# Kernel tuning notes

Measured on AMD Instinct MI355X. Metric: run time of the kernel, lower is better.

Reference implementation:

```python
import jax, jax.numpy as jnp
import numpy as np


def _bilinear(plane, coords):
    # plane: [B, C, H, W]; coords: [B, N, 2] in [-1, 1]; coords[...,0]->x (W axis), [...,1]->y (H axis)
    # matches F.grid_sample(mode='bilinear', padding_mode='border', align_corners=True)
    B, C, H, W = plane.shape
    x = jnp.clip((coords[..., 0] + 1.0) * 0.5 * (W - 1), 0.0, W - 1)
    y = jnp.clip((coords[..., 1] + 1.0) * 0.5 * (H - 1), 0.0, H - 1)
    x0 = jnp.floor(x)
    y0 = jnp.floor(y)
    x0i = x0.astype(jnp.int32)
    y0i = y0.astype(jnp.int32)
    x1i = jnp.minimum(x0i + 1, W - 1)
    y1i = jnp.minimum(y0i + 1, H - 1)
    wx = (x - x0)[:, :, None]
    wy = (y - y0)[:, :, None]
    pf = plane.reshape(B, C, H * W)

    def g(yi, xi):
        idx = (yi * W + xi)[:, None, :]            # [B,1,N]
        return jnp.take_along_axis(pf, idx, axis=2).transpose(0, 2, 1)  # [B,N,C]

    f00 = g(y0i, x0i)
    f01 = g(y0i, x1i)
    f10 = g(y1i, x0i)
    f11 = g(y1i, x1i)
    return (f00 * (1 - wx) * (1 - wy) + f01 * wx * (1 - wy)
            + f10 * (1 - wx) * wy + f11 * wx * wy)


def _sample(p, c_xz, c_xy, c_yz):
    # project 3D points onto the three canonical planes and sum bilinear features
    return (_bilinear(c_xz, p[..., jnp.array([0, 2])])
            + _bilinear(c_xy, p[..., jnp.array([0, 1])])
            + _bilinear(c_yz, p[..., jnp.array([1, 2])]))


def setup_inputs() -> dict:
    key = jax.random.key(0)
    ks = jax.random.split(key, 10)
    B, N, C, S, H = 8, 4096, 128, 8, 64
    query_pos = jax.random.uniform(ks[0], (B, N, 3), dtype=jnp.float32) * 2.0 - 1.0
    c_xz = jax.random.normal(ks[1], (B, C, H, H), dtype=jnp.float32)
    c_xy = jax.random.normal(ks[2], (B, C, H, H), dtype=jnp.float32)
    c_yz = jax.random.normal(ks[3], (B, C, H, H), dtype=jnp.float32)
    s = C ** -0.5
    Wq = jax.random.normal(ks[4], (C, C), dtype=jnp.float32) * s
    Wk = jax.random.normal(ks[5], (C, C), dtype=jnp.float32) * s
    Wv = jax.random.normal(ks[6], (C, C), dtype=jnp.float32) * s
    Wout = jax.random.normal(ks[7], (C, C), dtype=jnp.float32) * s
    Woff = jax.random.normal(ks[8], (C, 3 * S), dtype=jnp.float32) * s * 0.1  # small offsets
    return dict(query_pos=query_pos, c_xz=c_xz, c_xy=c_xy, c_yz=c_yz,
                Wq=Wq, bq=jnp.zeros((C,), jnp.float32),
                Wk=Wk, bk=jnp.zeros((C,), jnp.float32),
                Wv=Wv, bv=jnp.zeros((C,), jnp.float32),
                Wout=Wout, bout=jnp.zeros((C,), jnp.float32),
                Woff=Woff, boff=jnp.zeros((3 * S,), jnp.float32))


def reference(query_pos, c_xz, c_xy, c_yz, Wq, bq, Wk, bk, Wv, bv,
              Wout, bout, Woff, boff):
    B, N, _ = query_pos.shape
    C = Wq.shape[0]
    S = Woff.shape[1] // 3
    # sample features at query points (bilinear gather from triplanes)
    feature = _sample(query_pos, c_xz, c_xy, c_yz)                     # [B,N,C]
    # learned deformable offsets -> S auxiliary sample points per query
    offset = (feature @ Woff + boff).reshape(B, N, S, 3)
    aux_pts = offset + query_pos[:, :, None, :]                        # [B,N,S,3]
    aux_feat = _sample(aux_pts.reshape(B, N * S, 3),
                       c_xz, c_xy, c_yz).reshape(B, N, S, C)           # [B,N,S,C]
    k = aux_feat @ Wk + bk                                             # [B,N,S,C]
    v = aux_feat @ Wv + bv
    q = feature @ Wq + bq                                              # [B,N,C]
    scale = C ** (-0.5)
    q = q / scale  # faithful to original: q = q / self.scale
    sim = jnp.einsum('bnd,bnjd->bnj', q, k)                            # [B,N,S]
    attn = jax.nn.softmax(sim, axis=-1)
    out = jnp.einsum('bnj,bnjd->bnd', attn, v)                         # [B,N,C]
    out = out @ Wout + bout + feature                                  # residual
    return out
```

## Files before the change

kernel.cpp:

```cpp
#include <hip/hip_runtime.h>
#include <math.h>

#define BB 8
#define NN 4096
#define CC 128
#define SS 8
#define HH 64
#define HW 4096
#define PLANE_B (HW*CC)
#define SQRT_C 11.3137084989847603904f

__global__ __launch_bounds__(128) void transpose_planes(
    const float* __restrict__ pxz, const float* __restrict__ pxy,
    const float* __restrict__ pyz, float* __restrict__ dst) {
  int bid = blockIdx.x;
  int c   = threadIdx.x;
  int hw0 = (bid & 255) * 16;
  int b   = (bid >> 8) & 7;
  int p   = bid >> 11;
  const float* src = (p == 0) ? pxz : (p == 1) ? pxy : pyz;
  const float4* s4 = (const float4*)(src + (size_t)(b * CC + c) * HW + hw0);
  float4 v0 = s4[0], v1 = s4[1], v2 = s4[2], v3 = s4[3];
  float vals[16];
  vals[0]=v0.x; vals[1]=v0.y; vals[2]=v0.z; vals[3]=v0.w;
  vals[4]=v1.x; vals[5]=v1.y; vals[6]=v1.z; vals[7]=v1.w;
  vals[8]=v2.x; vals[9]=v2.y; vals[10]=v2.z; vals[11]=v2.w;
  vals[12]=v3.x; vals[13]=v3.y; vals[14]=v3.z; vals[15]=v3.w;
  float* d = dst + (size_t)(p * BB + b) * PLANE_B + (size_t)hw0 * CC + c;
#pragma unroll
  for (int i = 0; i < 16; ++i) d[i * CC] = vals[i];
}

__global__ __launch_bounds__(128) void prep_mats(
    const float* __restrict__ Wq, const float* __restrict__ bq,
    const float* __restrict__ Wk,
    const float* __restrict__ Wv, const float* __restrict__ bv,
    const float* __restrict__ Wout, const float* __restrict__ bout,
    const float* __restrict__ Woff,
    float* __restrict__ Mt, float* __restrict__ u,
    float* __restrict__ W2, float* __restrict__ b2,
    float* __restrict__ Wofft) {
  int t = threadIdx.x;
  int blk = blockIdx.x;
  if (blk < 128) {
    __shared__ float lwq[128];
    lwq[t] = Wq[blk * 128 + t];
    __syncthreads();
    float acc = 0.f;
#pragma unroll 8
    for (int d = 0; d < 128; ++d) acc += Wk[t * 128 + d] * lwq[d];
    Mt[blk * 128 + t] = SQRT_C * acc;
  } else if (blk < 256) {
    int c = blk - 128;
    float acc = 0.f;
#pragma unroll 8
    for (int e = 0; e < 128; ++e) acc += Wv[c * 128 + e] * Wout[e * 128 + t];
    W2[c * 128 + t] = acc;
  } else if (blk == 256) {
    float au = 0.f, ab = 0.f;
    for (int d = 0; d < 128; ++d) au += Wk[t * 128 + d] * bq[d];
    u[t] = SQRT_C * au;
    for (int e = 0; e < 128; ++e) ab += bv[e] * Wout[e * 128 + t];
    b2[t] = ab + bout[t];
  } else {
#pragma unroll
    for (int j = 0; j < 24; ++j) Wofft[j * 128 + t] = Woff[t * 24 + j];
  }
}

__device__ __forceinline__ void make_combo(float cx, float cy,
                                           int4* oi, float4* ow) {
  float fx = fminf(fmaxf((cx + 1.f) * 31.5f, 0.f), 63.f);
  float fy = fminf(fmaxf((cy + 1.f) * 31.5f, 0.f), 63.f);
  float x0f = floorf(fx), y0f = floorf(fy);
  int x0 = (int)x0f, y0 = (int)y0f;
  int x1 = min(x0 + 1, 63), y1 = min(y0 + 1, 63);
  float wx = fx - x0f, wy = fy - y0f;
  int r0 = y0 << 15, r1 = y1 << 15;
  int cb0 = x0 << 9, cb1 = x1 << 9;
  *oi = make_int4(r0 + cb0, r0 + cb1, r1 + cb0, r1 + cb1);
  float wxy = wx * wy;
  *ow = make_float4(1.f - wx - wy + wxy, wx - wxy, wy - wxy, wxy);
}

__device__ __forceinline__ float ldf(const char* p, int off) {
  return *(const float*)(p + off);
}

__global__ __launch_bounds__(128, 4) void deform_attn3(
    const float* __restrict__ qpos, const float* __restrict__ pT,
    const float* __restrict__ Mt, const float* __restrict__ u,
    const float* __restrict__ W2, const float* __restrict__ bias2,
    const float* __restrict__ Wofft, const float* __restrict__ boff,
    float* __restrict__ out) {
  const int tid = threadIdx.x;
  const int c = tid;
  const int l = tid & 63;
  const int wv = tid >> 6;
  const int bid = blockIdx.x;
  const int b = bid & 7;
  const int n0 = (bid >> 3) * 8;

  __shared__ float spos[24];
  __shared__ int4   sfi[24];
  __shared__ float4 sfw[24];
  __shared__ int4   sci[192];
  __shared__ float4 scw[192];
  __shared__ __align__(16) float sfeat[CC * 8];
  __shared__ __align__(16) float swacc[CC * 8];
  __shared__ float soff[8][24];
  __shared__ float sred[8][2][8];

  if (tid < 24) spos[tid] = qpos[(size_t)(b * NN + n0) * 3 + tid];
  __syncthreads();

  const char* pb0 = (const char*)(pT + (size_t)(0 * BB + b) * PLANE_B + c);
  const char* pb1 = (const char*)(pT + (size_t)(1 * BB + b) * PLANE_B + c);
  const char* pb2 = (const char*)(pT + (size_t)(2 * BB + b) * PLANE_B + c);

  if (tid < 24) {
    int p = tid >> 3, q = tid & 7;
    float px = spos[q * 3 + 0], py = spos[q * 3 + 1], pz = spos[q * 3 + 2];
    float cx = (p == 2) ? py : px;
    float cy = (p == 1) ? py : pz;
    make_combo(cx, cy, &sfi[tid], &sfw[tid]);
  }
  __syncthreads();

  float featr[8];
#pragma unroll
  for (int q = 0; q < 8; ++q) {
    float f = 0.f;
#pragma unroll
    for (int p = 0; p < 3; ++p) {
      int4 oi = sfi[p * 8 + q];
      float4 w = sfw[p * 8 + q];
      const char* base = (p == 0) ? pb0 : (p == 1) ? pb1 : pb2;
      f += w.x * ldf(base, oi.x) + w.y * ldf(base, oi.y)
         + w.z * ldf(base, oi.z) + w.w * ldf(base, oi.w);
    }
    featr[q] = f;
    sfeat[c * 8 + q] = f;
  }
  __syncthreads();

  float qk[8];
  {
    float uc = u[c];
#pragma unroll
    for (int q = 0; q < 8; ++q) qk[q] = uc;
#pragma unroll 4
    for (int cp = 0; cp < CC; ++cp) {
      float m = Mt[cp * CC + c];
      float4 f0 = *(const float4*)&sfeat[cp * 8];
      float4 f1 = *(const float4*)&sfeat[cp * 8 + 4];
      qk[0] += m * f0.x; qk[1] += m * f0.y; qk[2] += m * f0.z; qk[3] += m * f0.w;
      qk[4] += m * f1.x; qk[5] += m * f1.y; qk[6] += m * f1.z; qk[7] += m * f1.w;
    }
  }

#pragma unroll
  for (int rep = 0; rep < 2; ++rep) {
    int m = rep * 128 + tid;
    if (m < 192) {
      int q = m / 24;
      int t24 = m - q * 24;
      float acc = boff[t24];
      const float* wrow = Wofft + t24 * 128;
#pragma unroll 4
      for (int cp = 0; cp < CC; ++cp) acc += sfeat[cp * 8 + q] * wrow[cp];
      soff[q][t24] = acc;
    }
  }
  __syncthreads();

#pragma unroll
  for (int rep = 0; rep < 2; ++rep) {
    int m = rep * 128 + tid;
    if (m < 192) {
      int p = m >> 6, q = (m >> 3) & 7, j = m & 7;
      float ox = spos[q * 3 + 0] + soff[q][j * 3 + 0];
      float oy = spos[q * 3 + 1] + soff[q][j * 3 + 1];
      float oz = spos[q * 3 + 2] + soff[q][j * 3 + 2];
      float cx = (p == 2) ? oy : ox;
      float cy = (p == 1) ? oy : oz;
      make_combo(cx, cy, &sci[m], &scw[m]);
    }
  }
  __syncthreads();

  const int lb0 = l & 1, lb1 = (l >> 1) & 1, lb2 = (l >> 2) & 1;
#pragma unroll
  for (int q = 0; q < 8; ++q) {
    float a8[8], part[8];
#pragma unroll
    for (int j = 0; j < 8; ++j) {
      float a = 0.f;
#pragma unroll
      for (int p = 0; p < 3; ++p) {
        int idx = p * 64 + q * 8 + j;
        int4 oi = sci[idx];
        float4 w = scw[idx];
        const char* base = (p == 0) ? pb0 : (p == 1) ? pb1 : pb2;
        a += w.x * ldf(base, oi.x) + w.y * ldf(base, oi.y)
           + w.z * ldf(base, oi.z) + w.w * ldf(base, oi.w);
      }
      a8[j] = a;
      part[j] = a * qk[q];
    }
    float s2[4];
#pragma unroll
    for (int k = 0; k < 4; ++k) {
      float pa = part[2 * k], pb_ = part[2 * k + 1];
      float snd = lb0 ? pa : pb_;
      float kp  = lb0 ? pb_ : pa;
      s2[k] = kp + __shfl_xor(snd, 1);
    }
    float s4[2];
#pragma unroll
    for (int k = 0; k < 2; ++k) {
      float pa = s2[2 * k], pb_ = s2[2 * k + 1];
      float snd = lb1 ? pa : pb_;
      float kp  = lb1 ? pb_ : pa;
      s4[k] = kp + __shfl_xor(snd, 2);
    }
    float s8;
    {
      float snd = lb2 ? s4[0] : s4[1];
      float kp  = lb2 ? s4[1] : s4[0];
      s8 = kp + __shfl_xor(snd, 4);
    }
    s8 += __shfl_xor(s8, 8);
    s8 += __shfl_xor(s8, 16);
    s8 += __shfl_xor(s8, 32);
    if (l < 8) sred[q][wv][l] = s8;
    __syncthreads();
    float sim[8];
#pragma unroll
    for (int j = 0; j < 8; ++j) sim[j] = sred[q][0][j] + sred[q][1][j];
    float mx = fmaxf(fmaxf(fmaxf(sim[0], sim[1]), fmaxf(sim[2], sim[3])),
                     fmaxf(fmaxf(sim[4], sim[5]), fmaxf(sim[6], sim[7])));
    float den = 0.f;
#pragma unroll
    for (int j = 0; j < 8; ++j) { sim[j] = __expf(sim[j] - mx); den += sim[j]; }
    float inv = 1.f / den;
    float w = 0.f;
#pragma unroll
    for (int j = 0; j < 8; ++j) w += sim[j] * a8[j];
    swacc[c * 8 + q] = w * inv;
  }
  __syncthreads();

  float o[8];
  {
    float bb = bias2[c];
#pragma unroll
    for (int q = 0; q < 8; ++q) o[q] = bb;
#pragma unroll 4
    for (int cp = 0; cp < CC; ++cp) {
      float m = W2[cp * CC + c];
      float4 f0 = *(const float4*)&swacc[cp * 8];
      float4 f1 = *(const float4*)&swacc[cp * 8 + 4];
      o[0] += m * f0.x; o[1] += m * f0.y; o[2] += m * f0.z; o[3] += m * f0.w;
      o[4] += m * f1.x; o[5] += m * f1.y; o[6] += m * f1.z; o[7] += m * f1.w;
    }
  }
#pragma unroll
  for (int q = 0; q < 8; ++q) {
    out[(size_t)(b * NN + n0 + q) * CC + c] = o[q] + featr[q];
  }
}

__device__ __forceinline__ float bil(const float* __restrict__ base,
                                     float cx, float cy, int es, int rs) {
  float fx = fminf(fmaxf((cx + 1.f) * 31.5f, 0.f), 63.f);
  float fy = fminf(fmaxf((cy + 1.f) * 31.5f, 0.f), 63.f);
  float x0f = floorf(fx), y0f = floorf(fy);
  int x0 = (int)x0f, y0 = (int)y0f;
  int x1 = min(x0 + 1, 63), y1 = min(y0 + 1, 63);
  float wx = fx - x0f, wy = fy - y0f;
  const float* r0 = base + y0 * rs;
  const float* r1 = base + y1 * rs;
  float f00 = r0[x0 * es], f01 = r0[x1 * es];
  float f10 = r1[x0 * es], f11 = r1[x1 * es];
  float top = f00 + (f01 - f00) * wx;
  float bot = f10 + (f11 - f10) * wx;
  return top + (bot - top) * wy;
}

__global__ __launch_bounds__(128) void deform_attn_fb(
    const float* __restrict__ qpos,
    const float* __restrict__ pxz, const float* __restrict__ pxy,
    const float* __restrict__ pyz,
    const float* __restrict__ Mt, const float* __restrict__ u,
    const float* __restrict__ W2, const float* __restrict__ b2,
    const float* __restrict__ Woff, const float* __restrict__ boff,
    float* __restrict__ out) {
  const int tid = threadIdx.x;
  const int c = tid;
  const int bid = blockIdx.x;
  const int b = bid & 7;
  const int n0 = (bid >> 3) * 8;
  const int es = 1, rs = HH;
  const float* bxz = pxz + (size_t)(b * CC + c) * HW;
  const float* bxy = pxy + (size_t)(b * CC + c) * HW;
  const float* byz = pyz + (size_t)(b * CC + c) * HW;

  __shared__ __align__(16) float sfeat[CC * 8];
  __shared__ __align__(16) float swv[CC * 8];
  __shared__ float spos[24];
  __shared__ float soff[8][24];
  __shared__ float sred[8][2][8];

  if (tid < 24) spos[tid] = qpos[(size_t)(b * NN + n0) * 3 + tid];
  __syncthreads();
#pragma unroll
  for (int q = 0; q < 8; ++q) {
    float px = spos[q*3+0], py = spos[q*3+1], pz = spos[q*3+2];
    sfeat[c*8+q] = bil(bxz,px,pz,es,rs)+bil(bxy,px,py,es,rs)+bil(byz,py,pz,es,rs);
  }
  __syncthreads();
  float qk[8];
  {
    float uc = u[c];
#pragma unroll
    for (int q = 0; q < 8; ++q) qk[q] = uc;
    for (int cp = 0; cp < CC; ++cp) {
      float m = Mt[cp*CC+c];
#pragma unroll
      for (int q = 0; q < 8; ++q) qk[q] += m * sfeat[cp*8+q];
    }
  }
  if (tid < 120) {
    int q = tid/24, j = tid%24;
    float acc = boff[j];
    for (int cp = 0; cp < CC; ++cp) acc += sfeat[cp*8+q]*Woff[cp*24+j];
    soff[q][j] = acc;
  }
  if (tid < 72) {
    int q = 5+tid/24, j = tid%24;
    float acc = boff[j];
    for (int cp = 0; cp < CC; ++cp) acc += sfeat[cp*8+q]*Woff[cp*24+j];
    soff[q][j] = acc;
  }
  __syncthreads();
  const int wvid = tid >> 6;
  for (int q = 0; q < 8; ++q) {
    float px = spos[q*3+0], py = spos[q*3+1], pz = spos[q*3+2];
    float a8[8];
#pragma unroll
    for (int j = 0; j < 8; ++j) {
      float ox = px+soff[q][j*3+0], oy = py+soff[q][j*3+1], oz = pz+soff[q][j*3+2];
      float a = bil(bxz,ox,oz,es,rs)+bil(bxy,ox,oy,es,rs)+bil(byz,oy,oz,es,rs);
      a8[j] = a;
      float p = a * qk[q];
#pragma unroll
      for (int m = 1; m < 64; m <<= 1) p += __shfl_xor(p, m);
      if ((tid & 63) == 0) sred[q][wvid][j] = p;
    }
    __syncthreads();
    float attn[8], mx = -INFINITY;
#pragma unroll
    for (int j = 0; j < 8; ++j) { attn[j] = sred[q][0][j]+sred[q][1][j]; mx = fmaxf(mx, attn[j]); }
    float den = 0.f;
#pragma unroll
    for (int j = 0; j < 8; ++j) { attn[j] = __expf(attn[j]-mx); den += attn[j]; }
    float inv = 1.f/den, w = 0.f;
#pragma unroll
    for (int j = 0; j < 8; ++j) w += attn[j]*a8[j];
    swv[c*8+q] = w*inv;
  }
  __syncthreads();
  float o[8];
  {
    float bb = b2[c];
#pragma unroll
    for (int q = 0; q < 8; ++q) o[q] = bb;
    for (int cp = 0; cp < CC; ++cp) {
      float wv2 = W2[cp*CC+c];
#pragma unroll
      for (int q = 0; q < 8; ++q) o[q] += wv2 * swv[cp*8+q];
    }
  }
#pragma unroll
  for (int q = 0; q < 8; ++q)
    out[(size_t)(b*NN+n0+q)*CC+c] = o[q] + sfeat[c*8+q];
}

extern "C" void kernel_launch(void* const* d_in, const int* in_sizes, int n_in,
                              void* d_out, int out_size, void* d_ws, size_t ws_size,
                              hipStream_t stream) {
  const float* qpos = (const float*)d_in[0];
  const float* pxz  = (const float*)d_in[1];
  const float* pxy  = (const float*)d_in[2];
  const float* pyz  = (const float*)d_in[3];
  const float* Wq   = (const float*)d_in[4];
  const float* bq   = (const float*)d_in[5];
  const float* Wk   = (const float*)d_in[6];
  const float* Wv   = (const float*)d_in[8];
  const float* bv   = (const float*)d_in[9];
  const float* Wout = (const float*)d_in[10];
  const float* bout = (const float*)d_in[11];
  const float* Woff = (const float*)d_in[12];
  const float* boff = (const float*)d_in[13];
  float* out = (float*)d_out;

  float* w = (float*)d_ws;
  const size_t nT = (size_t)3 * BB * HW * CC;
  const size_t matFloats = 16384 + 128 + 16384 + 128 + 24 * 128;
  bool tp = ws_size >= (nT + matFloats) * sizeof(float);

  float* wsT  = w;
  float* wsMt = tp ? (w + nT) : w;
  float* wsU  = wsMt + 16384;
  float* wsW2 = wsU + 128;
  float* wsB2 = wsW2 + 16384;
  float* wsWofft = wsB2 + 128;

  prep_mats<<<258, 128, 0, stream>>>(Wq, bq, Wk, Wv, bv, Wout, bout, Woff,
                                     wsMt, wsU, wsW2, wsB2, wsWofft);
  if (tp) {
    transpose_planes<<<3 * BB * (HW / 16), 128, 0, stream>>>(pxz, pxy, pyz, wsT);
    deform_attn3<<<(BB * NN) / 8, 128, 0, stream>>>(
        qpos, wsT, wsMt, wsU, wsW2, wsB2, wsWofft, boff, out);
  } else {
    deform_attn_fb<<<(BB * NN) / 8, 128, 0, stream>>>(
        qpos, pxz, pxy, pyz, wsMt, wsU, wsW2, wsB2, Woff, boff, out);
  }
}
```

Before: 209.9 us.

## Split queries across waves with float2 channel gathers and in-wave softmax

The main kernel now has each wave handle 4 of the 8 queries, with each lane loading two adjacent channels as a float2 per bilinear corner. This halves the number of gather instructions and removes the per-query block barrier, since the softmax is now done entirely with intra-wave shuffles. qk values are staged through shared memory to match the new lane-to-channel layout. The Woff transpose in the prep kernel is dropped and Woff is read directly with strided access. The risks are extra shared-memory traffic and per-lane register pressure from holding two channel accumulators.

```diff
diff --git a/kernel.cpp b/kernel.cpp
--- a/kernel.cpp
+++ b/kernel.cpp
@@ -36,10 +36,8 @@
     const float* __restrict__ Wk,
     const float* __restrict__ Wv, const float* __restrict__ bv,
     const float* __restrict__ Wout, const float* __restrict__ bout,
-    const float* __restrict__ Woff,
     float* __restrict__ Mt, float* __restrict__ u,
-    float* __restrict__ W2, float* __restrict__ b2,
-    float* __restrict__ Wofft) {
+    float* __restrict__ W2, float* __restrict__ b2) {
   int t = threadIdx.x;
   int blk = blockIdx.x;
   if (blk < 128) {
@@ -56,15 +54,12 @@
 #pragma unroll 8
     for (int e = 0; e < 128; ++e) acc += Wv[c * 128 + e] * Wout[e * 128 + t];
     W2[c * 128 + t] = acc;
-  } else if (blk == 256) {
+  } else {
     float au = 0.f, ab = 0.f;
     for (int d = 0; d < 128; ++d) au += Wk[t * 128 + d] * bq[d];
     u[t] = SQRT_C * au;
     for (int e = 0; e < 128; ++e) ab += bv[e] * Wout[e * 128 + t];
     b2[t] = ab + bout[t];
-  } else {
-#pragma unroll
-    for (int j = 0; j < 24; ++j) Wofft[j * 128 + t] = Woff[t * 24 + j];
   }
 }
 
@@ -83,20 +78,21 @@
   *ow = make_float4(1.f - wx - wy + wxy, wx - wxy, wy - wxy, wxy);
 }
 
-__device__ __forceinline__ float ldf(const char* p, int off) {
-  return *(const float*)(p + off);
-}
-
-__global__ __launch_bounds__(128, 4) void deform_attn3(
+__device__ __forceinline__ float2 ld2(const char* p, int off) {
+  return *(const float2*)(p + off);
+}
+
+__global__ __launch_bounds__(128, 4) void deform_attn4(
     const float* __restrict__ qpos, const float* __restrict__ pT,
     const float* __restrict__ Mt, const float* __restrict__ u,
     const float* __restrict__ W2, const float* __restrict__ bias2,
-    const float* __restrict__ Wofft, const float* __restrict__ boff,
+    const float* __restrict__ Woff, const float* __restrict__ boff,
     float* __restrict__ out) {
   const int tid = threadIdx.x;
   const int c = tid;
   const int l = tid & 63;
   const int wv = tid >> 6;
+  const int qb = wv * 4;
   const int bid = blockIdx.x;
   const int b = bid & 7;
   const int n0 = (bid >> 3) * 8;
@@ -109,14 +105,13 @@
   __shared__ __align__(16) float sfeat[CC * 8];
   __shared__ __align__(16) float swacc[CC * 8];
   __shared__ float soff[8][24];
-  __shared__ float sred[8][2][8];
 
   if (tid < 24) spos[tid] = qpos[(size_t)(b * NN + n0) * 3 + tid];
   __syncthreads();
 
-  const char* pb0 = (const char*)(pT + (size_t)(0 * BB + b) * PLANE_B + c);
-  const char* pb1 = (const char*)(pT + (size_t)(1 * BB + b) * PLANE_B + c);
-  const char* pb2 = (const char*)(pT + (size_t)(2 * BB + b) * PLANE_B + c);
+  const char* gp0 = (const char*)(pT + (size_t)(0 * BB + b) * PLANE_B) + 8 * l;
+  const char* gp1 = (const char*)(pT + (size_t)(1 * BB + b) * PLANE_B) + 8 * l;
+  const char* gp2 = (const char*)(pT + (size_t)(2 * BB + b) * PLANE_B) + 8 * l;
 
   if (tid < 24) {
     int p = tid >> 3, q = tid & 7;
@@ -127,26 +122,33 @@
   }
   __syncthreads();
 
-  float featr[8];
-#pragma unroll
-  for (int q = 0; q < 8; ++q) {
-    float f = 0.f;
-#pragma unroll
-    for (int p = 0; p < 3; ++p) {
-      int4 oi = sfi[p * 8 + q];
-      float4 w = sfw[p * 8 + q];
-      const char* base = (p == 0) ? pb0 : (p == 1) ? pb1 : pb2;
-      f += w.x * ldf(base, oi.x) + w.y * ldf(base, oi.y)
-         + w.z * ldf(base, oi.z) + w.w * ldf(base, oi.w);
-    }
-    featr[q] = f;
-    sfeat[c * 8 + q] = f;
-  }
-  __syncthreads();
-
-  float qk[8];
+  {
+    float f0q[4], f1q[4];
+#pragma unroll
+    for (int qi = 0; qi < 4; ++qi) {
+      int q = qb + qi;
+      float f0 = 0.f, f1 = 0.f;
+#pragma unroll
+      for (int p = 0; p < 3; ++p) {
+        const char* g = (p == 0) ? gp0 : (p == 1) ? gp1 : gp2;
+        int4 oi = sfi[p * 8 + q];
+        float4 w = sfw[p * 8 + q];
+        float2 v;
+        v = ld2(g, oi.x); f0 += w.x * v.x; f1 += w.x * v.y;
+        v = ld2(g, oi.y); f0 += w.y * v.x; f1 += w.y * v.y;
+        v = ld2(g, oi.z); f0 += w.z * v.x; f1 += w.z * v.y;
+        v = ld2(g, oi.w); f0 += w.w * v.x; f1 += w.w * v.y;
+      }
+      f0q[qi] = f0; f1q[qi] = f1;
+    }
+    *(float4*)&sfeat[(2 * l) * 8 + qb]     = make_float4(f0q[0], f0q[1], f0q[2], f0q[3]);
+    *(float4*)&sfeat[(2 * l + 1) * 8 + qb] = make_float4(f1q[0], f1q[1], f1q[2], f1q[3]);
+  }
+  __syncthreads();
+
   {
     float uc = u[c];
+    float qk[8];
 #pragma unroll
     for (int q = 0; q < 8; ++q) qk[q] = uc;
 #pragma unroll 4
@@ -157,6 +159,8 @@
       qk[0] += m * f0.x; qk[1] += m * f0.y; qk[2] += m * f0.z; qk[3] += m * f0.w;
       qk[4] += m * f1.x; qk[5] += m * f1.y; qk[6] += m * f1.z; qk[7] += m * f1.w;
     }
+    *(float4*)&swacc[c * 8]     = make_float4(qk[0], qk[1], qk[2], qk[3]);
+    *(float4*)&swacc[c * 8 + 4] = make_float4(qk[4], qk[5], qk[6], qk[7]);
   }
 
 #pragma unroll
@@ -166,9 +170,8 @@
       int q = m / 24;
       int t24 = m - q * 24;
       float acc = boff[t24];
-      const float* wrow = Wofft + t24 * 128;
 #pragma unroll 4
-      for (int cp = 0; cp < CC; ++cp) acc += sfeat[cp * 8 + q] * wrow[cp];
+      for (int cp = 0; cp < CC; ++cp) acc += sfeat[cp * 8 + q] * Woff[cp * 24 + t24];
       soff[q][t24] = acc;
     }
   }
@@ -189,71 +192,87 @@
   }
   __syncthreads();
 
-  const int lb0 = l & 1, lb1 = (l >> 1) & 1, lb2 = (l >> 2) & 1;
-#pragma unroll
-  for (int q = 0; q < 8; ++q) {
-    float a8[8], part[8];
-#pragma unroll
-    for (int j = 0; j < 8; ++j) {
-      float a = 0.f;
-#pragma unroll
-      for (int p = 0; p < 3; ++p) {
-        int idx = p * 64 + q * 8 + j;
-        int4 oi = sci[idx];
-        float4 w = scw[idx];
-        const char* base = (p == 0) ? pb0 : (p == 1) ? pb1 : pb2;
-        a += w.x * ldf(base, oi.x) + w.y * ldf(base, oi.y)
-           + w.z * ldf(base, oi.z) + w.w * ldf(base, oi.w);
-      }
-      a8[j] = a;
-      part[j] = a * qk[q];
-    }
-    float s2[4];
-#pragma unroll
-    for (int k = 0; k < 4; ++k) {
-      float pa = part[2 * k], pb_ = part[2 * k + 1];
-      float snd = lb0 ? pa : pb_;
-      float kp  = lb0 ? pb_ : pa;
-      s2[k] = kp + __shfl_xor(snd, 1);
-    }
-    float s4[2];
-#pragma unroll
-    for (int k = 0; k < 2; ++k) {
-      float pa = s2[2 * k], pb_ = s2[2 * k + 1];
-      float snd = lb1 ? pa : pb_;
-      float kp  = lb1 ? pb_ : pa;
-      s4[k] = kp + __shfl_xor(snd, 2);
-    }
-    float s8;
-    {
-      float snd = lb2 ? s4[0] : s4[1];
-      float kp  = lb2 ? s4[1] : s4[0];
-      s8 = kp + __shfl_xor(snd, 4);
-    }
-    s8 += __shfl_xor(s8, 8);
-    s8 += __shfl_xor(s8, 16);
-    s8 += __shfl_xor(s8, 32);
-    if (l < 8) sred[q][wv][l] = s8;
-    __syncthreads();
-    float sim[8];
-#pragma unroll
-    for (int j = 0; j < 8; ++j) sim[j] = sred[q][0][j] + sred[q][1][j];
-    float mx = fmaxf(fmaxf(fmaxf(sim[0], sim[1]), fmaxf(sim[2], sim[3])),
-                     fmaxf(fmaxf(sim[4], sim[5]), fmaxf(sim[6], sim[7])));
-    float den = 0.f;
-#pragma unroll
-    for (int j = 0; j < 8; ++j) { sim[j] = __expf(sim[j] - mx); den += sim[j]; }
-    float inv = 1.f / den;
-    float w = 0.f;
-#pragma unroll
-    for (int j = 0; j < 8; ++j) w += sim[j] * a8[j];
-    swacc[c * 8 + q] = w * inv;
-  }
-  __syncthreads();
-
-  float o[8];
+  {
+    float4 qk0 = *(const float4*)&swacc[(2 * l) * 8 + qb];
+    float4 qk1 = *(const float4*)&swacc[(2 * l + 1) * 8 + qb];
+    const int lb0 = l & 1, lb1 = (l >> 1) & 1, lb2 = (l >> 2) & 1;
+    float w0q[4], w1q[4];
+#pragma unroll
+    for (int qi = 0; qi < 4; ++qi) {
+      int q = qb + qi;
+      float qv0 = (qi == 0) ? qk0.x : (qi == 1) ? qk0.y : (qi == 2) ? qk0.z : qk0.w;
+      float qv1 = (qi == 0) ? qk1.x : (qi == 1) ? qk1.y : (qi == 2) ? qk1.z : qk1.w;
+      float a0[8], a1[8], part[8];
+#pragma unroll
+      for (int j = 0; j < 8; ++j) {
+        float s0 = 0.f, s1 = 0.f;
+#pragma unroll
+        for (int p = 0; p < 3; ++p) {
+          int idx = p * 64 + q * 8 + j;
+          const char* g = (p == 0) ? gp0 : (p == 1) ? gp1 : gp2;
+          int4 oi = sci[idx];
+          float4 w = scw[idx];
+          float2 v;
+          v = ld2(g, oi.x); s0 += w.x * v.x; s1 += w.x * v.y;
+          v = ld2(g, oi.y); s0 += w.y * v.x; s1 += w.y * v.y;
+          v = ld2(g, oi.z); s0 += w.z * v.x; s1 += w.z * v.y;
+          v = ld2(g, oi.w); s0 += w.w * v.x; s1 += w.w * v.y;
+        }
+        a0[j] = s0; a1[j] = s1;
+        part[j] = s0 * qv0 + s1 * qv1;
+      }
+      float s2[4];
+#pragma unroll
+      for (int k = 0; k < 4; ++k) {
+        float pa = part[2 * k], pb_ = part[2 * k + 1];
+        float snd = lb0 ? pa : pb_;
+        float kp  = lb0 ? pb_ : pa;
+        s2[k] = kp + __shfl_xor(snd, 1);
+      }
+      float s4_[2];
+#pragma unroll
+      for (int k = 0; k < 2; ++k) {
+        float pa = s2[2 * k], pb_ = s2[2 * k + 1];
+        float snd = lb1 ? pa : pb_;
+        float kp  = lb1 ? pb_ : pa;
+        s4_[k] = kp + __shfl_xor(snd, 2);
+      }
+      float s8;
+      {
+        float snd = lb2 ? s4_[0] : s4_[1];
+        float kp  = lb2 ? s4_[1] : s4_[0];
+        s8 = kp + __shfl_xor(snd, 4);
+      }
+      s8 += __shfl_xor(s8, 8);
+      s8 += __shfl_xor(s8, 16);
+      s8 += __shfl_xor(s8, 32);
+      float mx = s8;
+      mx = fmaxf(mx, __shfl_xor(mx, 1));
+      mx = fmaxf(mx, __shfl_xor(mx, 2));
+      mx = fmaxf(mx, __shfl_xor(mx, 4));
+      float e = __expf(s8 - mx);
+      float den = e;
+      den += __shfl_xor(den, 1);
+      den += __shfl_xor(den, 2);
+      den += __shfl_xor(den, 4);
+      float attn = e / den;
+      float w0 = 0.f, w1 = 0.f;
+#pragma unroll
+      for (int j = 0; j < 8; ++j) {
+        float aj = __shfl(attn, j);
+        w0 += aj * a0[j];
+        w1 += aj * a1[j];
+      }
+      w0q[qi] = w0; w1q[qi] = w1;
+    }
+    *(float4*)&swacc[(2 * l) * 8 + qb]     = make_float4(w0q[0], w0q[1], w0q[2], w0q[3]);
+    *(float4*)&swacc[(2 * l + 1) * 8 + qb] = make_float4(w1q[0], w1q[1], w1q[2], w1q[3]);
+  }
+  __syncthreads();
+
   {
     float bb = bias2[c];
+    float o[8];
 #pragma unroll
     for (int q = 0; q < 8; ++q) o[q] = bb;
 #pragma unroll 4
@@ -264,10 +283,16 @@
       o[0] += m * f0.x; o[1] += m * f0.y; o[2] += m * f0.z; o[3] += m * f0.w;
       o[4] += m * f1.x; o[5] += m * f1.y; o[6] += m * f1.z; o[7] += m * f1.w;
     }
-  }
-#pragma unroll
-  for (int q = 0; q < 8; ++q) {
-    out[(size_t)(b * NN + n0 + q) * CC + c] = o[q] + featr[q];
+    float4 r0 = *(const float4*)&sfeat[c * 8];
+    float4 r1 = *(const float4*)&sfeat[c * 8 + 4];
+    out[(size_t)(b * NN + n0 + 0) * CC + c] = o[0] + r0.x;
+    out[(size_t)(b * NN + n0 + 1) * CC + c] = o[1] + r0.y;
+    out[(size_t)(b * NN + n0 + 2) * CC + c] = o[2] + r0.z;
+    out[(size_t)(b * NN + n0 + 3) * CC + c] = o[3] + r0.w;
+    out[(size_t)(b * NN + n0 + 4) * CC + c] = o[4] + r1.x;
+    out[(size_t)(b * NN + n0 + 5) * CC + c] = o[5] + r1.y;
+    out[(size_t)(b * NN + n0 + 6) * CC + c] = o[6] + r1.z;
+    out[(size_t)(b * NN + n0 + 7) * CC + c] = o[7] + r1.w;
   }
 }
 
@@ -407,7 +432,7 @@
 
   float* w = (float*)d_ws;
   const size_t nT = (size_t)3 * BB * HW * CC;
-  const size_t matFloats = 16384 + 128 + 16384 + 128 + 24 * 128;
+  const size_t matFloats = 16384 + 128 + 16384 + 128;
   bool tp = ws_size >= (nT + matFloats) * sizeof(float);
 
   float* wsT  = w;
@@ -415,14 +440,13 @@
   float* wsU  = wsMt + 16384;
   float* wsW2 = wsU + 128;
   float* wsB2 = wsW2 + 16384;
-  float* wsWofft = wsB2 + 128;
-
-  prep_mats<<<258, 128, 0, stream>>>(Wq, bq, Wk, Wv, bv, Wout, bout, Woff,
-                                     wsMt, wsU, wsW2, wsB2, wsWofft);
+
+  prep_mats<<<257, 128, 0, stream>>>(Wq, bq, Wk, Wv, bv, Wout, bout,
+                                     wsMt, wsU, wsW2, wsB2);
   if (tp) {
     transpose_planes<<<3 * BB * (HW / 16), 128, 0, stream>>>(pxz, pxy, pyz, wsT);
-    deform_attn3<<<(BB * NN) / 8, 128, 0, stream>>>(
-        qpos, wsT, wsMt, wsU, wsW2, wsB2, wsWofft, boff, out);
+    deform_attn4<<<(BB * NN) / 8, 128, 0, stream>>>(
+        qpos, wsT, wsMt, wsU, wsW2, wsB2, Woff, boff, out);
   } else {
     deform_attn_fb<<<(BB * NN) / 8, 128, 0, stream>>>(
         qpos, pxz, pxy, pyz, wsMt, wsU, wsW2, wsB2, Woff, boff, out);
```

Result: slower. 737.8 us (+251.6%).
